# Kernel tuning notes

Measured on AMD Instinct MI355X. Metric: run time of the kernel, lower is better.

## Reference

```python
import jax, jax.numpy as jnp
import numpy as np

B, S, D = 16, 1024, 768
H = 12
HD = D // H  # 64


def setup_inputs() -> dict:
    key = jax.random.key(0)
    ks = jax.random.split(key, 9)
    s = 1.0 / np.sqrt(D)
    x = jax.random.normal(ks[0], (B, S, D), dtype=jnp.float32)
    Wq = jax.random.uniform(ks[1], (H, HD, D), minval=-s, maxval=s, dtype=jnp.float32)
    bq = jax.random.uniform(ks[2], (H, HD), minval=-s, maxval=s, dtype=jnp.float32)
    Wk = jax.random.uniform(ks[3], (H, HD, D), minval=-s, maxval=s, dtype=jnp.float32)
    bk = jax.random.uniform(ks[4], (H, HD), minval=-s, maxval=s, dtype=jnp.float32)
    Wv = jax.random.uniform(ks[5], (H, HD, D), minval=-s, maxval=s, dtype=jnp.float32)
    bv = jax.random.uniform(ks[6], (H, HD), minval=-s, maxval=s, dtype=jnp.float32)
    Wo = jax.random.uniform(ks[7], (D, D), minval=-s, maxval=s, dtype=jnp.float32)
    bo = jax.random.uniform(ks[8], (D,), minval=-s, maxval=s, dtype=jnp.float32)
    return {"x": x, "Wq": Wq, "bq": bq, "Wk": Wk, "bk": bk,
            "Wv": Wv, "bv": bv, "Wo": Wo, "bo": bo}


def reference(x, Wq, bq, Wk, bk, Wv, bv, Wo, bo):
    # per-head projections: [B,S,D] x [H,HD,D] -> [B,H,S,HD]
    q = jnp.einsum('bsd,hed->bhse', x, Wq) + bq[None, :, None, :]
    k = jnp.einsum('bsd,hed->bhse', x, Wk) + bk[None, :, None, :]
    v = jnp.einsum('bsd,hed->bhse', x, Wv) + bv[None, :, None, :]
    scores = jnp.einsum('bhse,bhte->bhst', q, k) / jnp.sqrt(jnp.float32(HD))
    weights = jax.nn.softmax(scores, axis=-1)  # [B,H,S,S]
    attn = jnp.einsum('bhst,bhte->bhse', weights, v)  # [B,H,S,HD]
    # concat heads along last dim (head order matches torch.cat)
    concat = attn.transpose(0, 2, 1, 3).reshape(B, S, H * HD)
    out = concat @ Wo.T + bo
    return out
```

## Files before the change

kernel.cpp:

```cpp
#include <hip/hip_runtime.h>
#include <hip/hip_bf16.h>

typedef unsigned short u16;
typedef unsigned int u32;
typedef __attribute__((ext_vector_type(2))) unsigned int u32x2;
typedef __attribute__((ext_vector_type(4))) unsigned int u32x4;
typedef __attribute__((ext_vector_type(4))) float f32x4;
typedef __attribute__((ext_vector_type(16))) float f32x16;
typedef __attribute__((ext_vector_type(8))) short s16x8;
typedef __attribute__((ext_vector_type(4))) unsigned short u16x4;
typedef __attribute__((ext_vector_type(8))) unsigned short u16x8;

#define QSCALE 0.18033688011112042f

#define BARRIER() do { __builtin_amdgcn_s_barrier(); __builtin_amdgcn_sched_barrier(0); } while (0)
#define WAIT_VM0() do { asm volatile("s_waitcnt vmcnt(0)" ::: "memory"); __builtin_amdgcn_sched_barrier(0); } while (0)

__device__ inline u16 f2bf(float f) {
  union { float f; unsigned u; } x; x.f = f;
  unsigned r = x.u + 0x7FFFu + ((x.u >> 16) & 1u);
  return (u16)(r >> 16);
}

__device__ inline u32 cvtpk(float lo, float hi) {
  u32 r;
  asm("v_cvt_pk_bf16_f32 %0, %1, %2" : "=v"(r) : "v"(lo), "v"(hi));
  return r;
}

__device__ inline void pl32swap(u32& a, u32& b) {
  asm("v_permlane32_swap_b32 %0, %1" : "+v"(a), "+v"(b));
}

__global__ void cvt_all(const float* __restrict__ x,
                        const float* __restrict__ Wq, const float* __restrict__ Wk,
                        const float* __restrict__ Wv, const float* __restrict__ Wo,
                        const float* __restrict__ bq, const float* __restrict__ bk,
                        const float* __restrict__ bv,
                        u16* __restrict__ xb, u16* __restrict__ wqkv,
                        u16* __restrict__ wo, float* __restrict__ bqkv) {
  int i = blockIdx.x * blockDim.x + threadIdx.x;
  const int NX = 3145728;
  const int NW = 147456;
  if (i < NX) {
    const float4 v = ((const float4*)x)[i];
    u16x4 o; o[0] = f2bf(v.x); o[1] = f2bf(v.y); o[2] = f2bf(v.z); o[3] = f2bf(v.w);
    ((u16x4*)xb)[i] = o;
    return;
  }
  i -= NX;
  if (i < 4 * NW) {
    const int w = i / NW, k = i - w * NW;
    const float* s = (w == 0) ? Wq : (w == 1) ? Wk : (w == 2) ? Wv : Wo;
    u16* d = (w == 3) ? wo : wqkv + (size_t)w * 589824;
    const float4 v = ((const float4*)s)[k];
    u16x4 o; o[0] = f2bf(v.x); o[1] = f2bf(v.y); o[2] = f2bf(v.z); o[3] = f2bf(v.w);
    ((u16x4*)d)[k] = o;
    return;
  }
  i -= 4 * NW;
  if (i < 576) {
    const int w = i / 192, k = i - w * 192;
    const float* s = (w == 0) ? bq : (w == 1) ? bk : bv;
    ((float4*)bqkv)[w * 192 + k] = ((const float4*)s)[k];
  }
}

template<int FR, int STORE_BF16, int QKV_SCALE>
__global__ __launch_bounds__(512, 2) void gemm8(
    const u16* __restrict__ A, const u16* __restrict__ Bm,
    const float* __restrict__ bias, void* __restrict__ C,
    int N, int K, int ntiles)
{
  constexpr int BM = FR * 32;
  constexpr int ASZ = BM * 128;
  constexpr int BUF = ASZ + 32768;
  __shared__ char lds[2 * BUF];

  const int tid = threadIdx.x, wave = tid >> 6, lane = tid & 63;
  const int il = lane & 15, g = lane >> 4;
  const int Lr = lane >> 3, Lc = lane & 7;
  const int wm = wave >> 2, wn = wave & 3;

  const int cpx = (int)gridDim.x >> 3;
  const int orig = (blockIdx.x & 7) * cpx + (blockIdx.x >> 3);
  const int tm = (orig / ntiles) * BM, tn = (orig % ntiles) * 256;

  const size_t Kb = (size_t)K * 2;
  const int colb = (Lc * 16) ^ (Lr << 4);

  auto stageA = [&](int buf, int half, int k0) {
    char* db = &lds[buf * BUF + half * 16384 + wave * 1024];
#pragma unroll
    for (int q = 0; q < 2; ++q) {
      const int row = tm + half * 128 + q * 64 + wave * 8 + Lr;
      const char* src = (const char*)A + (size_t)row * Kb + k0 * 2 + colb;
      __builtin_amdgcn_global_load_lds((const __attribute__((address_space(1))) void*)src,
          (__attribute__((address_space(3))) void*)(db + q * 8192), 16, 0, 0);
    }
  };
  auto stageB = [&](int buf, int half, int k0) {
    char* db = &lds[buf * BUF + ASZ + half * 16384 + wave * 1024];
#pragma unroll
    for (int q = 0; q < 2; ++q) {
      const int row = tn + half * 128 + q * 64 + wave * 8 + Lr;
      const char* src = (const char*)Bm + (size_t)row * Kb + k0 * 2 + colb;
      __builtin_amdgcn_global_load_lds((const __attribute__((address_space(1))) void*)src,
          (__attribute__((address_space(3))) void*)(db + q * 8192), 16, 0, 0);
    }
  };
  auto ldA = [&](int buf, int fr, int kk) -> s16x8 {
    const int row = wm * (FR * 16) + fr * 16 + il;
    const int cb = (kk * 64 + g * 16) ^ ((il & 7) << 4);
    return *(const s16x8*)&lds[buf * BUF + row * 128 + cb];
  };
  auto ldB = [&](int buf, int fc, int kk) -> s16x8 {
    const int row = wn * 64 + fc * 16 + il;
    const int cb = (kk * 64 + g * 16) ^ ((il & 7) << 4);
    return *(const s16x8*)&lds[buf * BUF + ASZ + row * 128 + cb];
  };

  f32x4 acc[FR][4] = {};
  const int nK = K >> 6;

#pragma unroll
  for (int h = 0; h < FR / 4; ++h) stageA(0, h, 0);
  stageB(0, 0, 0); stageB(0, 1, 0);
  WAIT_VM0();
  BARRIER();

  for (int t = 0; t < nK; ++t) {
    const int cur = t & 1, nxt = cur ^ 1;
    const int k1 = (t + 1) << 6;
    const bool pf = (t + 1 < nK);

    s16x8 bf[4][2];
#pragma unroll
    for (int fc = 0; fc < 4; ++fc) { bf[fc][0] = ldB(cur, fc, 0); bf[fc][1] = ldB(cur, fc, 1); }

#pragma unroll
    for (int p = 0; p < FR / 2; ++p) {
      s16x8 a00 = ldA(cur, 2 * p, 0),     a01 = ldA(cur, 2 * p, 1);
      s16x8 a10 = ldA(cur, 2 * p + 1, 0), a11 = ldA(cur, 2 * p + 1, 1);
      if (p == 0 && pf) {
#pragma unroll
        for (int h = 0; h < FR / 4; ++h) stageA(nxt, h, k1);
      }
      if (p == 1 && pf) { stageB(nxt, 0, k1); stageB(nxt, 1, k1); }
      BARRIER();
      __builtin_amdgcn_s_setprio(1);
#pragma unroll
      for (int fc = 0; fc < 4; ++fc) {
        acc[2*p][fc]   = __builtin_amdgcn_mfma_f32_16x16x32_bf16(a00, bf[fc][0], acc[2*p][fc], 0, 0, 0);
        acc[2*p][fc]   = __builtin_amdgcn_mfma_f32_16x16x32_bf16(a01, bf[fc][1], acc[2*p][fc], 0, 0, 0);
        acc[2*p+1][fc] = __builtin_amdgcn_mfma_f32_16x16x32_bf16(a10, bf[fc][0], acc[2*p+1][fc], 0, 0, 0);
        acc[2*p+1][fc] = __builtin_amdgcn_mfma_f32_16x16x32_bf16(a11, bf[fc][1], acc[2*p+1][fc], 0, 0, 0);
      }
      __builtin_amdgcn_s_setprio(0);
      if (p == FR / 2 - 1 && pf) WAIT_VM0();
      BARRIER();
    }
  }

#pragma unroll
  for (int fr = 0; fr < FR; ++fr) {
    const int row0 = tm + wm * (FR * 16) + fr * 16 + g * 4;
#pragma unroll
    for (int fc = 0; fc < 4; ++fc) {
      const int col = tn + wn * 64 + fc * 16 + il;
      const float bb = bias[col];
#pragma unroll
      for (int r = 0; r < 4; ++r) {
        float v = acc[fr][fc][r] + bb;
        if (QKV_SCALE) { if (col < 768) v *= QSCALE; }
        if (STORE_BF16) ((u16*)C)[(size_t)(row0 + r) * N + col] = f2bf(v);
        else            ((float*)C)[(size_t)(row0 + r) * N + col] = v;
      }
    }
  }
}

__global__ __launch_bounds__(256) void transpose_v(const u16* __restrict__ qkv,
                                                   u16* __restrict__ vT) {
  __shared__ u16 T[64 * 64];
  const int kt = blockIdx.x, h = blockIdx.y, b = blockIdx.z;
  const int t = threadIdx.x;
  {
    const int k = t >> 2, c = (t & 3) * 16;
    const u16* src = qkv + (size_t)(b * 1024 + kt * 64 + k) * 2304 + 1536 + h * 64 + c;
    const int sw = ((k >> 3) & 7) << 4;
#pragma unroll
    for (int s2 = 0; s2 < 2; ++s2) {
      s16x8 v = *(const s16x8*)(src + s2 * 8);
      *(s16x8*)((char*)T + k * 128 + (((c + s2 * 8) * 2) ^ sw)) = v;
    }
  }
  __syncthreads();
  const int w = t >> 6, l = t & 63;
  const int kj = (l & 7) * 8;
  const int sw = (l & 7) << 4;
#pragma unroll
  for (int i = 0; i < 2; ++i) {
    const int e = w * 16 + i * 8 + (l >> 3);
    u16x8 o;
#pragma unroll
    for (int j = 0; j < 8; ++j)
      o[j] = *(const u16*)((const char*)T + (kj + j) * 128 + ((e * 2) ^ sw));
    *(u16x8*)(vT + ((size_t)(b * 12 + h) * 64 + e) * 1024 + kt * 64 + kj) = o;
  }
}

__global__ __launch_bounds__(256) void attn_fwd(const u16* __restrict__ qkv,
                                                const u16* __restrict__ vT,
                                                u16* __restrict__ concat)
{
  __shared__ u16 Kl[64 * 64];
  __shared__ u16 Vl[64 * 64];

  const int tid = threadIdx.x, wave = tid >> 6, lane = tid & 63;
  const int wg = blockIdx.x;
  const int bh = (wg & 7) | ((wg >> 6) << 3);
  const int qb = (wg >> 3) & 7;
  const int b = bh / 12, h = bh % 12;
  const int q = lane & 31, hi = lane >> 5;
  const int qs0 = qb * 128 + wave * 32;

  const char* qkvB = (const char*)qkv;
  const size_t rowB = (size_t)b * 1024 * 4608;
  const char* vtB = (const char*)vT + (size_t)bh * 64 * 2048;

  s16x8 qf[4];
  {
    const char* qp = qkvB + rowB + (size_t)(qs0 + q) * 4608 + h * 128 + hi * 16;
#pragma unroll
    for (int s = 0; s < 4; ++s) qf[s] = *(const s16x8*)(qp + s * 32);
  }

  float l_ = 0.f;
  f32x16 accO[2] = {};

  const int Lr = lane >> 3, Lc = lane & 7;
  const int colb = (Lc * 16) ^ ((Lr & 7) << 4);
  const int swk = (q & 7) << 4;

  for (int kv0 = 0; kv0 < 1024; kv0 += 64) {
#pragma unroll
    for (int i = 0; i < 2; ++i) {
      const int row = wave * 16 + i * 8 + Lr;
      const char* ks = qkvB + rowB + (size_t)(kv0 + row) * 4608 + 1536 + h * 128 + colb;
      __builtin_amdgcn_global_load_lds((const __attribute__((address_space(1))) void*)ks,
          (__attribute__((address_space(3))) void*)(Kl + (wave * 16 + i * 8) * 64), 16, 0, 0);
      const char* vs = vtB + (size_t)row * 2048 + kv0 * 2 + colb;
      __builtin_amdgcn_global_load_lds((const __attribute__((address_space(1))) void*)vs,
          (__attribute__((address_space(3))) void*)(Vl + (wave * 16 + i * 8) * 64), 16, 0, 0);
    }
    __syncthreads();

    f32x16 st[2] = {};
    __builtin_amdgcn_s_setprio(1);
#pragma unroll
    for (int s = 0; s < 4; ++s) {
      const int cb = (s * 32 + hi * 16) ^ swk;
      s16x8 k0 = *(const s16x8*)((const char*)Kl + q * 128 + cb);
      s16x8 k1 = *(const s16x8*)((const char*)Kl + (32 + q) * 128 + cb);
      st[0] = __builtin_amdgcn_mfma_f32_32x32x16_bf16(k0, qf[s], st[0], 0, 0, 0);
      st[1] = __builtin_amdgcn_mfma_f32_32x32x16_bf16(k1, qf[s], st[1], 0, 0, 0);
    }
    __builtin_amdgcn_s_setprio(0);

    float cs0 = 0.f, cs1 = 0.f;
#pragma unroll
    for (int r = 0; r < 16; ++r) {
      const float p0 = __builtin_amdgcn_exp2f(st[0][r]);
      const float p1 = __builtin_amdgcn_exp2f(st[1][r]);
      st[0][r] = p0; st[1][r] = p1;
      cs0 += p0; cs1 += p1;
    }
    l_ += cs0 + cs1;

    s16x8 pa[4];
#pragma unroll
    for (int kb = 0; kb < 2; ++kb)
#pragma unroll
      for (int ks = 0; ks < 2; ++ks) {
        u32 A0 = cvtpk(st[kb][ks * 8 + 0], st[kb][ks * 8 + 1]);
        u32 A1 = cvtpk(st[kb][ks * 8 + 2], st[kb][ks * 8 + 3]);
        u32 B0 = cvtpk(st[kb][ks * 8 + 4], st[kb][ks * 8 + 5]);
        u32 B1 = cvtpk(st[kb][ks * 8 + 6], st[kb][ks * 8 + 7]);
        pl32swap(A0, B0);
        pl32swap(A1, B1);
        u32x4 w = {A0, A1, B0, B1};
        pa[kb * 2 + ks] = __builtin_bit_cast(s16x8, w);
      }

    __builtin_amdgcn_s_setprio(1);
#pragma unroll
    for (int ksub = 0; ksub < 4; ++ksub) {
      const int cb = (ksub * 32 + hi * 16) ^ swk;
      s16x8 v0 = *(const s16x8*)((const char*)Vl + q * 128 + cb);
      s16x8 v1 = *(const s16x8*)((const char*)Vl + (32 + q) * 128 + cb);
      accO[0] = __builtin_amdgcn_mfma_f32_32x32x16_bf16(v0, pa[ksub], accO[0], 0, 0, 0);
      accO[1] = __builtin_amdgcn_mfma_f32_32x32x16_bf16(v1, pa[ksub], accO[1], 0, 0, 0);
    }
    __builtin_amdgcn_s_setprio(0);
    __syncthreads();
  }

  l_ += __shfl_xor(l_, 32);
  const float linv = __builtin_amdgcn_rcpf(l_);
  u16* crow = concat + ((size_t)b * 1024 + qs0 + q) * 768 + h * 64;
#pragma unroll
  for (int eb = 0; eb < 2; ++eb)
#pragma unroll
    for (int rq = 0; rq < 4; ++rq) {
      u32 w0 = cvtpk(accO[eb][rq * 4 + 0] * linv, accO[eb][rq * 4 + 1] * linv);
      u32 w1 = cvtpk(accO[eb][rq * 4 + 2] * linv, accO[eb][rq * 4 + 3] * linv);
      u32x2 w = {w0, w1};
      *(u16x4*)(crow + eb * 32 + rq * 8 + hi * 4) = __builtin_bit_cast(u16x4, w);
    }
}

extern "C" void kernel_launch(void* const* d_in, const int* in_sizes, int n_in,
                              void* d_out, int out_size, void* d_ws, size_t ws_size,
                              hipStream_t stream) {
  const float* x  = (const float*)d_in[0];
  const float* Wq = (const float*)d_in[1];
  const float* bq = (const float*)d_in[2];
  const float* Wk = (const float*)d_in[3];
  const float* bk = (const float*)d_in[4];
  const float* Wv = (const float*)d_in[5];
  const float* bv = (const float*)d_in[6];
  const float* Wo = (const float*)d_in[7];
  const float* bo = (const float*)d_in[8];

  const size_t XN = (size_t)16384 * 768;
  const size_t WN = (size_t)768 * 768;

  u16* xb   = (u16*)d_ws;
  u16* wqkv = xb + XN;
  u16* wo   = wqkv + 3 * WN;
  float* bqkv = (float*)(wo + WN);
  u16* qkv  = (u16*)(bqkv + 2304);
  u16* vt   = qkv + (size_t)16384 * 2304;
  u16* cc   = xb;

  cvt_all<<<(3736128 + 255) / 256, 256, 0, stream>>>(
      x, Wq, Wk, Wv, Wo, bq, bk, bv, xb, wqkv, wo, bqkv);

  gemm8<8, 1, 1><<<576, 512, 0, stream>>>(xb, wqkv, bqkv, qkv, 2304, 768, 9);

  transpose_v<<<dim3(16, 12, 16), 256, 0, stream>>>(qkv, vt);

  attn_fwd<<<1536, 256, 0, stream>>>(qkv, vt, cc);

  gemm8<4, 0, 0><<<384, 512, 0, stream>>>(cc, wo, bo, d_out, 768, 768, 3);
}
```

Baseline: 208.9 us.

## Retile GEMMs to fixed 256-row M tiles with templated narrower N tiles

Reworks the GEMM kernel so every block covers a fixed 256-row M tile and a variable N tile of FC*64 columns, replacing the earlier variable-M, fixed-256-N layout. Staging of A and B is merged into one routine issued at the start of each K step. Both GEMMs switch to 256x192 tiles: the QKV GEMM goes from 576 to 768 blocks and the output projection from 384 to 256 blocks. The new shape changes load balance across CUs, LDS footprint and the ratio of A to B reuse.

```diff
diff --git a/kernel.cpp b/kernel.cpp
--- a/kernel.cpp
+++ b/kernel.cpp
@@ -66,15 +66,15 @@
   }
 }
 
-template<int FR, int STORE_BF16, int QKV_SCALE>
+template<int FC, int STORE_BF16, int QKV_SCALE>
 __global__ __launch_bounds__(512, 2) void gemm8(
     const u16* __restrict__ A, const u16* __restrict__ Bm,
     const float* __restrict__ bias, void* __restrict__ C,
     int N, int K, int ntiles)
 {
-  constexpr int BM = FR * 32;
-  constexpr int ASZ = BM * 128;
-  constexpr int BUF = ASZ + 32768;
+  constexpr int ASZ = 32768;
+  constexpr int BSZ = FC * 8192;
+  constexpr int BUF = ASZ + BSZ;
   __shared__ char lds[2 * BUF];
 
   const int tid = threadIdx.x, wave = tid >> 6, lane = tid & 63;
@@ -84,90 +84,80 @@
 
   const int cpx = (int)gridDim.x >> 3;
   const int orig = (blockIdx.x & 7) * cpx + (blockIdx.x >> 3);
-  const int tm = (orig / ntiles) * BM, tn = (orig % ntiles) * 256;
+  const int tm = (orig / ntiles) * 256, tn = (orig % ntiles) * (FC * 64);
 
   const size_t Kb = (size_t)K * 2;
   const int colb = (Lc * 16) ^ (Lr << 4);
 
-  auto stageA = [&](int buf, int half, int k0) {
-    char* db = &lds[buf * BUF + half * 16384 + wave * 1024];
-#pragma unroll
-    for (int q = 0; q < 2; ++q) {
-      const int row = tm + half * 128 + q * 64 + wave * 8 + Lr;
+  auto stageAll = [&](int buf, int k0) {
+    char* base = &lds[buf * BUF];
+#pragma unroll
+    for (int c = 0; c < 4; ++c) {
+      const int row = tm + c * 64 + wave * 8 + Lr;
       const char* src = (const char*)A + (size_t)row * Kb + k0 * 2 + colb;
       __builtin_amdgcn_global_load_lds((const __attribute__((address_space(1))) void*)src,
-          (__attribute__((address_space(3))) void*)(db + q * 8192), 16, 0, 0);
-    }
-  };
-  auto stageB = [&](int buf, int half, int k0) {
-    char* db = &lds[buf * BUF + ASZ + half * 16384 + wave * 1024];
-#pragma unroll
-    for (int q = 0; q < 2; ++q) {
-      const int row = tn + half * 128 + q * 64 + wave * 8 + Lr;
+          (__attribute__((address_space(3))) void*)(base + c * 8192 + wave * 1024), 16, 0, 0);
+    }
+#pragma unroll
+    for (int c = 0; c < FC; ++c) {
+      const int row = tn + c * 64 + wave * 8 + Lr;
       const char* src = (const char*)Bm + (size_t)row * Kb + k0 * 2 + colb;
       __builtin_amdgcn_global_load_lds((const __attribute__((address_space(1))) void*)src,
-          (__attribute__((address_space(3))) void*)(db + q * 8192), 16, 0, 0);
+          (__attribute__((address_space(3))) void*)(base + ASZ + c * 8192 + wave * 1024), 16, 0, 0);
     }
   };
   auto ldA = [&](int buf, int fr, int kk) -> s16x8 {
-    const int row = wm * (FR * 16) + fr * 16 + il;
+    const int row = wm * 128 + fr * 16 + il;
     const int cb = (kk * 64 + g * 16) ^ ((il & 7) << 4);
     return *(const s16x8*)&lds[buf * BUF + row * 128 + cb];
   };
   auto ldB = [&](int buf, int fc, int kk) -> s16x8 {
-    const int row = wn * 64 + fc * 16 + il;
+    const int row = wn * (FC * 16) + fc * 16 + il;
     const int cb = (kk * 64 + g * 16) ^ ((il & 7) << 4);
     return *(const s16x8*)&lds[buf * BUF + ASZ + row * 128 + cb];
   };
 
-  f32x4 acc[FR][4] = {};
+  f32x4 acc[8][FC] = {};
   const int nK = K >> 6;
 
-#pragma unroll
-  for (int h = 0; h < FR / 4; ++h) stageA(0, h, 0);
-  stageB(0, 0, 0); stageB(0, 1, 0);
+  stageAll(0, 0);
   WAIT_VM0();
   BARRIER();
 
   for (int t = 0; t < nK; ++t) {
-    const int cur = t & 1, nxt = cur ^ 1;
-    const int k1 = (t + 1) << 6;
+    const int cur = t & 1;
     const bool pf = (t + 1 < nK);
 
-    s16x8 bf[4][2];
-#pragma unroll
-    for (int fc = 0; fc < 4; ++fc) { bf[fc][0] = ldB(cur, fc, 0); bf[fc][1] = ldB(cur, fc, 1); }
-
-#pragma unroll
-    for (int p = 0; p < FR / 2; ++p) {
+    s16x8 bfr[FC][2];
+#pragma unroll
+    for (int fc = 0; fc < FC; ++fc) { bfr[fc][0] = ldB(cur, fc, 0); bfr[fc][1] = ldB(cur, fc, 1); }
+
+#pragma unroll
+    for (int p = 0; p < 4; ++p) {
       s16x8 a00 = ldA(cur, 2 * p, 0),     a01 = ldA(cur, 2 * p, 1);
       s16x8 a10 = ldA(cur, 2 * p + 1, 0), a11 = ldA(cur, 2 * p + 1, 1);
-      if (p == 0 && pf) {
-#pragma unroll
-        for (int h = 0; h < FR / 4; ++h) stageA(nxt, h, k1);
-      }
-      if (p == 1 && pf) { stageB(nxt, 0, k1); stageB(nxt, 1, k1); }
+      if (p == 0 && pf) stageAll(cur ^ 1, (t + 1) << 6);
       BARRIER();
       __builtin_amdgcn_s_setprio(1);
 #pragma unroll
-      for (int fc = 0; fc < 4; ++fc) {
-        acc[2*p][fc]   = __builtin_amdgcn_mfma_f32_16x16x32_bf16(a00, bf[fc][0], acc[2*p][fc], 0, 0, 0);
-        acc[2*p][fc]   = __builtin_amdgcn_mfma_f32_16x16x32_bf16(a01, bf[fc][1], acc[2*p][fc], 0, 0, 0);
-        acc[2*p+1][fc] = __builtin_amdgcn_mfma_f32_16x16x32_bf16(a10, bf[fc][0], acc[2*p+1][fc], 0, 0, 0);
-        acc[2*p+1][fc] = __builtin_amdgcn_mfma_f32_16x16x32_bf16(a11, bf[fc][1], acc[2*p+1][fc], 0, 0, 0);
+      for (int fc = 0; fc < FC; ++fc) {
+        acc[2*p][fc]   = __builtin_amdgcn_mfma_f32_16x16x32_bf16(a00, bfr[fc][0], acc[2*p][fc], 0, 0, 0);
+        acc[2*p][fc]   = __builtin_amdgcn_mfma_f32_16x16x32_bf16(a01, bfr[fc][1], acc[2*p][fc], 0, 0, 0);
+        acc[2*p+1][fc] = __builtin_amdgcn_mfma_f32_16x16x32_bf16(a10, bfr[fc][0], acc[2*p+1][fc], 0, 0, 0);
+        acc[2*p+1][fc] = __builtin_amdgcn_mfma_f32_16x16x32_bf16(a11, bfr[fc][1], acc[2*p+1][fc], 0, 0, 0);
       }
       __builtin_amdgcn_s_setprio(0);
-      if (p == FR / 2 - 1 && pf) WAIT_VM0();
+      if (p == 3 && pf) WAIT_VM0();
       BARRIER();
     }
   }
 
 #pragma unroll
-  for (int fr = 0; fr < FR; ++fr) {
-    const int row0 = tm + wm * (FR * 16) + fr * 16 + g * 4;
-#pragma unroll
-    for (int fc = 0; fc < 4; ++fc) {
-      const int col = tn + wn * 64 + fc * 16 + il;
+  for (int fr = 0; fr < 8; ++fr) {
+    const int row0 = tm + wm * 128 + fr * 16 + g * 4;
+#pragma unroll
+    for (int fc = 0; fc < FC; ++fc) {
+      const int col = tn + wn * (FC * 16) + fc * 16 + il;
       const float bb = bias[col];
 #pragma unroll
       for (int r = 0; r < 4; ++r) {
@@ -347,11 +337,11 @@
   cvt_all<<<(3736128 + 255) / 256, 256, 0, stream>>>(
       x, Wq, Wk, Wv, Wo, bq, bk, bv, xb, wqkv, wo, bqkv);
 
-  gemm8<8, 1, 1><<<576, 512, 0, stream>>>(xb, wqkv, bqkv, qkv, 2304, 768, 9);
+  gemm8<3, 1, 1><<<768, 512, 0, stream>>>(xb, wqkv, bqkv, qkv, 2304, 768, 12);
 
   transpose_v<<<dim3(16, 12, 16), 256, 0, stream>>>(qkv, vt);
 
   attn_fwd<<<1536, 256, 0, stream>>>(qkv, vt, cc);
 
-  gemm8<4, 0, 0><<<384, 512, 0, stream>>>(cc, wo, bo, d_out, 768, 768, 3);
-}
+  gemm8<3, 0, 0><<<256, 512, 0, stream>>>(cc, wo, bo, d_out, 768, 768, 4);
+}
```

After: 191.8 us. -8.2%, faster.
